# Kernel optimization log

Hardware: AMD Instinct MI355X
Metric: run time of the kernel (lower is better)

Reference implementation:

```python
import jax, jax.numpy as jnp
import numpy as np

B, S, T, K = 96, 4, 16, 36           # groups, fixed 4 slots, max tags per slot, num boxes
V_DIM, Q_DIM, H = 1024, 512, 512


def setup_inputs() -> dict:
    key = jax.random.key(0)
    k_v, k_q, k_m, k_w1, k_b1, k_w2, k_b2 = jax.random.split(key, 7)

    # deterministic ragged lengths in [1, T], cyclic -> sum is exact
    lengths = (np.arange(B * S) % T) + 1              # [B*S], sum = 24 * 136 = 3264
    N = int(lengths.sum())                            # total rows in v / q
    # binary tag-attention mask: first `len` positions set per slot
    tags_attention = (np.arange(T)[None, :] < lengths[:, None]).astype(np.int32)
    tags_attention = jnp.asarray(tags_attention.reshape(B, S, T))

    v = jax.random.normal(k_v, (N, K, V_DIM), dtype=jnp.float32)
    q = jax.random.normal(k_q, (N, Q_DIM), dtype=jnp.float32)

    # box mask: random 0/1 but guarantee at least one valid box per group
    box_mask = (jax.random.uniform(k_m, (B, K)) < 0.9).astype(jnp.float32)
    box_mask = box_mask.at[:, 0].set(1.0)

    # FCNet (weight-normed Linear + ReLU; dropout inactive at eval) and scoring Linear
    w1 = jax.random.normal(k_w1, (V_DIM + Q_DIM, H), dtype=jnp.float32) * 0.02
    b1 = jax.random.normal(k_b1, (H,), dtype=jnp.float32) * 0.02
    w2 = jax.random.normal(k_w2, (H,), dtype=jnp.float32) * 0.02
    b2 = jax.random.normal(k_b2, (), dtype=jnp.float32) * 0.02

    return {"v": v, "q": q, "box_mask": box_mask, "tags_attention": tags_attention,
            "w1": w1, "b1": b1, "w2": w2, "b2": b2}


def reference(v, q, box_mask, tags_attention, w1, b1, w2, b2):
    N, Kb, _ = v.shape
    # logits: concat(v, q repeated over boxes) -> ReLU FC -> scalar score per box
    vq = jnp.concatenate([v, jnp.broadcast_to(q[:, None, :], (N, Kb, q.shape[-1]))], axis=-1)
    joint = jax.nn.relu(jnp.einsum('nkd,dh->nkh', vq, w1) + b1)      # [N, K, H]
    logits = jnp.einsum('nkh,h->nk', joint, w2) + b2                 # [N, K]

    # pad_sequence: ragged rows -> [B, S, T, K] via vectorized gather
    Bg, Sg, Tg = tags_attention.shape
    lengths = tags_attention.sum(-1).reshape(-1)                     # [B*S]
    starts = jnp.cumsum(lengths) - lengths                           # exclusive cumsum
    idx = starts[:, None] + jnp.arange(Tg)                           # [B*S, T]
    valid = jnp.arange(Tg)[None, :] < lengths[:, None]               # [B*S, T]
    gathered = jnp.take(logits, jnp.clip(idx, 0, N - 1), axis=0)     # [B*S, T, K]
    padded = jnp.where(valid[..., None], gathered, 0.0).reshape(Bg, Sg, Tg, Kb)

    # masked_softmax (allennlp-style) over the box dim with box_mask [B,1,1,K]
    mask = box_mask[:, None, None, :]
    s = jax.nn.softmax(padded * mask, axis=-1) * mask
    w = s / (s.sum(axis=-1, keepdims=True) + 1e-13)
    return w
```

## Files before the change

kernel.cpp:

```cpp
#include <hip/hip_runtime.h>
#include <hip/hip_bf16.h>
#include <cstdint>
#include <cstddef>

#define BB 96
#define SS 4
#define TT 16
#define KK 36
#define VDIM 1024
#define QDIM 512
#define HH 512
#define W1R 1536
#define NROWS 3264
#define MM (NROWS * KK)

typedef __attribute__((ext_vector_type(8))) short short8;
typedef __attribute__((ext_vector_type(4))) float f32x4;

static __device__ __forceinline__ unsigned short f2bf(float f) {
    union { float f; unsigned u; } v; v.f = f;
    unsigned u = v.u;
    u += 0x7FFFu + ((u >> 16) & 1u);
    return (unsigned short)(u >> 16);
}

static __device__ __forceinline__ unsigned pk2(float lo, float hi) {
    __hip_bfloat162 h = __float22bfloat162_rn(make_float2(lo, hi));
    union { __hip_bfloat162 h; unsigned u; } cv;
    cv.h = h;
    return cv.u;
}

__device__ __forceinline__ void gload_lds16(const void* g, void* l) {
    __builtin_amdgcn_global_load_lds(
        (const __attribute__((address_space(1))) unsigned int*)g,
        (__attribute__((address_space(3))) unsigned int*)l, 16, 0, 0);
}

#define SB() __builtin_amdgcn_sched_barrier(0)

__global__ __launch_bounds__(256) void prep_w1T(const float* __restrict__ w1,
                                                unsigned short* __restrict__ w1T) {
    __shared__ float tile[64][65];
    int k0 = blockIdx.x * 64;
    int c0 = blockIdx.y * 64;
    int li = threadIdx.x & 63;
    int gi = threadIdx.x >> 6;
#pragma unroll
    for (int r = 0; r < 64; r += 4)
        tile[r + gi][li] = w1[(size_t)(k0 + r + gi) * HH + c0 + li];
    __syncthreads();
#pragma unroll
    for (int r = 0; r < 64; r += 4) {
        int c = r + gi;
        w1T[(size_t)(c0 + c) * W1R + k0 + li] = f2bf(tile[li][c]);
    }
}

__global__ __launch_bounds__(512) void starts_kernel(const int* __restrict__ tags,
                                                     int* __restrict__ starts,
                                                     int* __restrict__ lengths) {
    __shared__ int sl[BB * SS];
    int tid = threadIdx.x;
    int len = 0;
    if (tid < BB * SS) {
#pragma unroll
        for (int i = 0; i < TT; ++i) len += tags[tid * TT + i];
        sl[tid] = len;
    }
    __syncthreads();
    for (int off = 1; off < BB * SS; off <<= 1) {
        int v = 0;
        if (tid < BB * SS && tid >= off) v = sl[tid - off];
        __syncthreads();
        if (tid < BB * SS) sl[tid] += v;
        __syncthreads();
    }
    if (tid < BB * SS) { starts[tid] = sl[tid] - len; lengths[tid] = len; }
}

__global__ __launch_bounds__(256, 3) void qproj_mfma(const float* __restrict__ q,
                                                     const unsigned short* __restrict__ w1T,
                                                     const float* __restrict__ b1,
                                                     float* __restrict__ qp) {
    __shared__ __align__(16) unsigned short At[2][64 * 64];
    __shared__ __align__(16) unsigned short Bt[2][128 * 64];

    int tid = threadIdx.x, lane = tid & 63, wid = tid >> 6;
    int wm = wid >> 1, wn = wid & 1;
    int bx = blockIdx.x;
    int nb = bx & 3, mb = bx >> 2;
    int n0q = mb * 64, cb = nb * 128;
    int lr = lane & 15, lg = lane >> 4;

    const float* a_base = q + (size_t)(n0q + wid * 16 + (lane >> 4)) * QDIM + (lane & 15) * 4;
    const unsigned short* b_base = w1T + (size_t)(cb + wid * 32 + (lane >> 3)) * W1R + 1024
                                 + (((lane & 7) ^ (lane >> 3)) * 8);

    f32x4 acc[2][4];
#pragma unroll
    for (int mt = 0; mt < 2; ++mt)
#pragma unroll
        for (int nt = 0; nt < 4; ++nt) acc[mt][nt] = (f32x4){0.f, 0.f, 0.f, 0.f};

#define QP_CVT_WRITE(DST, AR)                                                  \
    _Pragma("unroll") for (int p = 0; p < 4; ++p) {                            \
        int r = wid * 16 + (lane >> 4) + p * 4;                                \
        int boff = r * 128 + ((((lane & 15) * 8)) ^ ((r & 7) << 4));           \
        uint2 d;                                                               \
        d.x = pk2(AR[p].x, AR[p].y);                                           \
        d.y = pk2(AR[p].z, AR[p].w);                                           \
        *(uint2*)((char*)(DST) + boff) = d;                                    \
    }

#define QP_COMPUTE(AC, BC)                                                     \
    _Pragma("unroll") for (int kk = 0; kk < 2; ++kk) {                         \
        short8 af[2], bf[4];                                                   \
        _Pragma("unroll") for (int mt = 0; mt < 2; ++mt) {                     \
            int R = wm * 32 + mt * 16 + lr;                                    \
            int off = R * 128 + ((kk * 64 + lg * 16) ^ ((R & 7) << 4));        \
            af[mt] = *(const short8*)((const char*)(AC) + off);                \
        }                                                                      \
        _Pragma("unroll") for (int nt = 0; nt < 4; ++nt) {                     \
            int R = wn * 64 + nt * 16 + lr;                                    \
            int off = R * 128 + ((kk * 64 + lg * 16) ^ ((R & 7) << 4));        \
            bf[nt] = *(const short8*)((const char*)(BC) + off);                \
        }                                                                      \
        __builtin_amdgcn_s_setprio(1);                                         \
        _Pragma("unroll") for (int mt = 0; mt < 2; ++mt)                       \
            _Pragma("unroll") for (int nt = 0; nt < 4; ++nt)                   \
                acc[mt][nt] = __builtin_amdgcn_mfma_f32_16x16x32_bf16(         \
                    af[mt], bf[nt], acc[mt][nt], 0, 0, 0);                     \
        __builtin_amdgcn_s_setprio(0);                                         \
    }

    {
        float4 ar[4];
#pragma unroll
        for (int p = 0; p < 4; ++p) ar[p] = *(const float4*)(a_base + (size_t)p * 4 * QDIM);
#pragma unroll
        for (int o = 0; o < 4; ++o)
            gload_lds16(b_base + (size_t)o * 8 * W1R, &Bt[0][(wid * 32 + o * 8) * 64]);
        SB();
        QP_CVT_WRITE(&At[0][0], ar)
    }
#pragma unroll 1
    for (int t = 0; t < 7; ++t) {
        int k0 = (t + 1) * 64;
        const unsigned short* Ac = &At[t & 1][0];
        const unsigned short* Bc = &Bt[t & 1][0];
        unsigned short* An = &At[(t + 1) & 1][0];
        unsigned short* Bn = &Bt[(t + 1) & 1][0];
        float4 ar[4];
#pragma unroll
        for (int p = 0; p < 4; ++p)
            ar[p] = *(const float4*)(a_base + (size_t)p * 4 * QDIM + k0);
#pragma unroll
        for (int o = 0; o < 4; ++o)
            gload_lds16(b_base + (size_t)o * 8 * W1R + k0, &Bn[(wid * 32 + o * 8) * 64]);
        SB();
        asm volatile("s_waitcnt vmcnt(8)" ::: "memory");
        asm volatile("s_waitcnt lgkmcnt(0)" ::: "memory");
        __builtin_amdgcn_s_barrier();
        SB();
        QP_COMPUTE(Ac, Bc)
        SB();
        QP_CVT_WRITE(An, ar)
    }
    SB();
    asm volatile("s_waitcnt vmcnt(0)" ::: "memory");
    asm volatile("s_waitcnt lgkmcnt(0)" ::: "memory");
    __builtin_amdgcn_s_barrier();
    SB();
    QP_COMPUTE(&At[1][0], &Bt[1][0])
#undef QP_COMPUTE
#undef QP_CVT_WRITE

#pragma unroll
    for (int nt = 0; nt < 4; ++nt) {
        int c = cb + wn * 64 + nt * 16 + lr;
        float b1v = b1[c];
#pragma unroll
        for (int mt = 0; mt < 2; ++mt)
#pragma unroll
            for (int r = 0; r < 4; ++r) {
                int row = wm * 32 + mt * 16 + lg * 4 + r;
                qp[(size_t)(n0q + row) * HH + c] = acc[mt][nt][r] + b1v;
            }
    }
}

__global__ __launch_bounds__(512, 2) void main_gemm(const float* __restrict__ v,
                                                    const unsigned short* __restrict__ w1T,
                                                    const float* __restrict__ qp,
                                                    const float* __restrict__ w2,
                                                    float* __restrict__ logits2) {
    __shared__ __align__(16) unsigned short At[2][16384];
    __shared__ __align__(16) unsigned short Bt[2][16384];

    int tid = threadIdx.x, lane = tid & 63, wid = tid >> 6;
    int wm = wid >> 2, wn = wid & 3;
    int bx = blockIdx.x;
    int xcd = bx & 7;
    int base = (xcd < 6) ? xcd * 115 : 690 + (xcd - 6) * 114;
    int orig = base + (bx >> 3);
    int ch = orig & 1, mb = orig >> 1;
    int m0 = mb * 256, cb = ch * 256;
    int lr = lane & 15, lg = lane >> 4;

    const float* a_base = v + (size_t)(m0 + wid * 32 + (lane >> 4)) * VDIM + (lane & 15) * 4;
    const unsigned short* b_base = w1T + (size_t)(cb + wid * 32 + (lane >> 3)) * W1R
                                 + (((lane & 7) ^ (lane >> 3)) * 8);

    f32x4 acc[8][4];
#pragma unroll
    for (int mt = 0; mt < 8; ++mt)
#pragma unroll
        for (int nt = 0; nt < 4; ++nt) acc[mt][nt] = (f32x4){0.f, 0.f, 0.f, 0.f};

#define MG_CVT_WRITE(AN, AR)                                                   \
    _Pragma("unroll") for (int p = 0; p < 8; ++p) {                            \
        int r = wid * 32 + (lane >> 4) + p * 4;                                \
        int boff = r * 128 + ((((lane & 15) * 8)) ^ ((r & 7) << 4));           \
        uint2 d;                                                               \
        d.x = pk2(AR[p].x, AR[p].y);                                           \
        d.y = pk2(AR[p].z, AR[p].w);                                           \
        *(uint2*)((char*)(AN) + boff) = d;                                     \
    }

#define MG_READ_A8(AF, AC, MTB)                                                \
    _Pragma("unroll") for (int mt = 0; mt < 4; ++mt)                           \
        _Pragma("unroll") for (int kk = 0; kk < 2; ++kk) {                     \
            int R = wm * 128 + ((MTB) + mt) * 16 + lr;                         \
            int off = R * 128 + ((kk * 64 + lg * 16) ^ ((R & 7) << 4));        \
            AF[mt * 2 + kk] = *(const short8*)((const char*)(AC) + off);       \
        }

#define MG_READ_B8(BF, BC)                                                     \
    _Pragma("unroll") for (int nt = 0; nt < 4; ++nt)                           \
        _Pragma("unroll") for (int kk = 0; kk < 2; ++kk) {                     \
            int C = wn * 64 + nt * 16 + lr;                                    \
            int off = C * 128 + ((kk * 64 + lg * 16) ^ ((C & 7) << 4));        \
            BF[nt * 2 + kk] = *(const short8*)((const char*)(BC) + off);       \
        }

#define MG_MFMA32(AF, BF, MTB)                                                 \
    __builtin_amdgcn_s_setprio(1);                                             \
    _Pragma("unroll") for (int mt = 0; mt < 4; ++mt)                           \
        _Pragma("unroll") for (int nt = 0; nt < 4; ++nt)                       \
            _Pragma("unroll") for (int kk = 0; kk < 2; ++kk)                   \
                acc[(MTB) + mt][nt] = __builtin_amdgcn_mfma_f32_16x16x32_bf16( \
                    AF[mt * 2 + kk], BF[nt * 2 + kk], acc[(MTB) + mt][nt],     \
                    0, 0, 0);                                                  \
    __builtin_amdgcn_s_setprio(0);

#define BODY(T, AC, AN, BC, BN, VM)                                            \
  do {                                                                         \
    float4 ar[8];                                                              \
    if ((T) < 15) {                                                            \
        const int kA = ((T) + 1) * 64;                                         \
        _Pragma("unroll") for (int p = 0; p < 8; ++p)                          \
            ar[p] = *(const float4*)(a_base + (size_t)p * 4 * VDIM + kA);      \
    }                                                                          \
    SB();                                                                      \
    asm volatile("s_waitcnt vmcnt(" VM ")" ::: "memory");     \
    asm volatile("s_waitcnt lgkmcnt(0)" ::: "memory");    \
    __builtin_amdgcn_s_barrier();                                              \
    SB();                                                                      \
    if ((T) < 15) {       \
        const int kB = ((T) + 1) * 64;                                         \
        _Pragma("unroll") for (int o = 0; o < 4; ++o)                          \
            gload_lds16(b_base + (size_t)o * 8 * W1R + kB,                     \
                        (BN) + (wid * 32 + o * 8) * 64);                       \
    }                                                                          \
    SB();                                                                      \
    {                                                                          \
        short8 af0[8], bfv[8];                                                 \
        MG_READ_A8(af0, AC, 0)                                                 \
        MG_READ_B8(bfv, BC)                                                    \
        MG_MFMA32(af0, bfv, 0)                                                 \
        short8 af1[8];                                                         \
        MG_READ_A8(af1, AC, 4)                                                 \
        MG_MFMA32(af1, bfv, 4)                                                 \
    }                                                                          \
    SB();                                                                      \
    if ((T) < 15) { MG_CVT_WRITE(AN, ar) }         \
  } while (0)

    {
        float4 ar[8];
#pragma unroll
        for (int p = 0; p < 8; ++p) ar[p] = *(const float4*)(a_base + (size_t)p * 4 * VDIM);
#pragma unroll
        for (int o = 0; o < 4; ++o)
            gload_lds16(b_base + (size_t)o * 8 * W1R, &Bt[0][(wid * 32 + o * 8) * 64]);
        SB();
        MG_CVT_WRITE(At[0], ar)
    }

#pragma unroll 1
    for (int tt = 0; tt < 14; tt += 2) {
        BODY(tt,     At[0], At[1], Bt[0], Bt[1], "8");
        BODY(tt + 1, At[1], At[0], Bt[1], Bt[0], "8");
    }
    BODY(14, At[0], At[1], Bt[0], Bt[1], "8");
    BODY(15, At[1], At[0], Bt[1], Bt[0], "0");
#undef BODY
#undef MG_MFMA32
#undef MG_READ_A8
#undef MG_READ_B8
#undef MG_CVT_WRITE

    __syncthreads();
    float* qs = (float*)&At[0][0];
    float* fl = qs + 9 * 256;
    int n0 = m0 / KK;
    for (int i = tid; i < 9 * 256; i += 512) {
        int nn = n0 + (i >> 8);
        if (nn >= NROWS) nn = NROWS - 1;
        qs[i] = qp[(size_t)nn * HH + cb + (i & 255)];
    }
    __syncthreads();

    float part[8][4] = {{0.f}};
#pragma unroll
    for (int nt = 0; nt < 4; ++nt) {
        int c = wn * 64 + nt * 16 + lr;
        float w2v = w2[cb + c];
#pragma unroll
        for (int mt = 0; mt < 8; ++mt)
#pragma unroll
            for (int r = 0; r < 4; ++r) {
                int row = wm * 128 + mt * 16 + lg * 4 + r;
                int ni = (m0 + row) / KK - n0;
                float pre = acc[mt][nt][r] + qs[ni * 256 + c];
                part[mt][r] += fmaxf(pre, 0.f) * w2v;
            }
    }
#pragma unroll
    for (int mt = 0; mt < 8; ++mt)
#pragma unroll
        for (int r = 0; r < 4; ++r) {
            float s = part[mt][r];
            s += __shfl_xor(s, 1, 64);
            s += __shfl_xor(s, 2, 64);
            s += __shfl_xor(s, 4, 64);
            s += __shfl_xor(s, 8, 64);
            if (lr == 0) fl[wn * 256 + wm * 128 + mt * 16 + lg * 4 + r] = s;
        }
    __syncthreads();
    if (tid < 256)
        logits2[(size_t)ch * MM + m0 + tid] =
            fl[tid] + fl[256 + tid] + fl[512 + tid] + fl[768 + tid];
}

__global__ __launch_bounds__(256) void softmax_kernel(const float* __restrict__ logits2,
                                                      const float* __restrict__ box_mask,
                                                      const int* __restrict__ starts,
                                                      const int* __restrict__ lengths,
                                                      float* __restrict__ out) {
    int lane = threadIdx.x & 63;
    int g = blockIdx.x * 4 + (threadIdx.x >> 6);
    int t   = g & (TT - 1);
    int row = g >> 4;
    int b   = row >> 2;

    int length = lengths[row];
    int start  = starts[row];

    int k = lane;
    bool kv = k < KK;
    float mval = kv ? box_mask[b * KK + k] : 0.f;
    bool act = kv && (mval != 0.f);

    float l = 0.f;
    if (act && t < length) {
        size_t idx = (size_t)(start + t) * KK + k;
        l = logits2[idx] + logits2[MM + idx];
    }

    float lm = act ? l : -1e30f;
#pragma unroll
    for (int off = 32; off >= 1; off >>= 1) lm = fmaxf(lm, __shfl_xor(lm, off, 64));

    float e = act ? expf(l - lm) : 0.f;
    float se = e;
#pragma unroll
    for (int off = 32; off >= 1; off >>= 1) se += __shfl_xor(se, off, 64);

    if (kv) out[(size_t)g * KK + k] = e / se;
}

extern "C" void kernel_launch(void* const* d_in, const int* in_sizes, int n_in,
                              void* d_out, int out_size, void* d_ws, size_t ws_size,
                              hipStream_t stream) {
    const float* v        = (const float*)d_in[0];
    const float* q        = (const float*)d_in[1];
    const float* box_mask = (const float*)d_in[2];
    const int*   tags     = (const int*)d_in[3];
    const float* w1       = (const float*)d_in[4];
    const float* b1       = (const float*)d_in[5];
    const float* w2       = (const float*)d_in[6];

    char* ws = (char*)d_ws;
    unsigned short* w1T   = (unsigned short*)ws;
    float* qp      = (float*)(ws + 1572864);
    float* logits2 = (float*)(ws + 1572864 + 6684672);
    int*   starts  = (int*)(ws + 1572864 + 6684672 + 940032);
    int*   lengths = (int*)(ws + 1572864 + 6684672 + 940032 + 1536);
    float* out     = (float*)d_out;

    hipLaunchKernelGGL(prep_w1T, dim3(24, 8), dim3(256), 0, stream, w1, w1T);
    hipLaunchKernelGGL(starts_kernel, dim3(1), dim3(512), 0, stream, tags, starts, lengths);
    hipLaunchKernelGGL(qproj_mfma, dim3((NROWS / 64) * 4), dim3(256), 0, stream,
                       q, w1T, b1, qp);
    hipLaunchKernelGGL(main_gemm, dim3((MM / 256) * 2), dim3(512), 0, stream,
                       v, w1T, qp, w2, logits2);
    hipLaunchKernelGGL(softmax_kernel, dim3((BB * SS * TT) / 4), dim3(256), 0, stream,
                       logits2, box_mask, starts, lengths, out);
}
```

Before: 252.4 us.

## Restructure GEMM main loop into eight-phase ping-pong schedule with split prefetches

```diff
diff --git a/kernel.cpp b/kernel.cpp
--- a/kernel.cpp
+++ b/kernel.cpp
@@ -218,6 +218,12 @@
 #pragma unroll
         for (int nt = 0; nt < 4; ++nt) acc[mt][nt] = (f32x4){0.f, 0.f, 0.f, 0.f};
 
+    float4 ar[8];
+
+#define MG_LOADA(AR, KA)                                                       \
+    _Pragma("unroll") for (int p = 0; p < 8; ++p)                              \
+        AR[p] = *(const float4*)(a_base + (size_t)p * 4 * VDIM + (KA));
+
 #define MG_CVT_WRITE(AN, AR)                                                   \
     _Pragma("unroll") for (int p = 0; p < 8; ++p) {                            \
         int r = wid * 32 + (lane >> 4) + p * 4;                                \
@@ -228,14 +234,6 @@
         *(uint2*)((char*)(AN) + boff) = d;                                     \
     }
 
-#define MG_READ_A8(AF, AC, MTB)                                                \
-    _Pragma("unroll") for (int mt = 0; mt < 4; ++mt)                           \
-        _Pragma("unroll") for (int kk = 0; kk < 2; ++kk) {                     \
-            int R = wm * 128 + ((MTB) + mt) * 16 + lr;                         \
-            int off = R * 128 + ((kk * 64 + lg * 16) ^ ((R & 7) << 4));        \
-            AF[mt * 2 + kk] = *(const short8*)((const char*)(AC) + off);       \
-        }
-
 #define MG_READ_B8(BF, BC)                                                     \
     _Pragma("unroll") for (int nt = 0; nt < 4; ++nt)                           \
         _Pragma("unroll") for (int kk = 0; kk < 2; ++kk) {                     \
@@ -244,72 +242,127 @@
             BF[nt * 2 + kk] = *(const short8*)((const char*)(BC) + off);       \
         }
 
-#define MG_MFMA32(AF, BF, MTB)                                                 \
+#define MG_READ_AQ(AF, AC, Q)                                                  \
+    _Pragma("unroll") for (int j = 0; j < 2; ++j)                              \
+        _Pragma("unroll") for (int kk = 0; kk < 2; ++kk) {                     \
+            int R = wm * 128 + (2 * (Q) + j) * 16 + lr;                        \
+            int off = R * 128 + ((kk * 64 + lg * 16) ^ ((R & 7) << 4));        \
+            AF[j * 2 + kk] = *(const short8*)((const char*)(AC) + off);        \
+        }
+
+#define MG_MFMA16(AF, BFV, Q)                                                  \
     __builtin_amdgcn_s_setprio(1);                                             \
-    _Pragma("unroll") for (int mt = 0; mt < 4; ++mt)                           \
+    _Pragma("unroll") for (int j = 0; j < 2; ++j)                              \
         _Pragma("unroll") for (int nt = 0; nt < 4; ++nt)                       \
             _Pragma("unroll") for (int kk = 0; kk < 2; ++kk)                   \
-                acc[(MTB) + mt][nt] = __builtin_amdgcn_mfma_f32_16x16x32_bf16( \
-                    AF[mt * 2 + kk], BF[nt * 2 + kk], acc[(MTB) + mt][nt],     \
-                    0, 0, 0);                                                  \
+                acc[2 * (Q) + j][nt] =                                         \
+                    __builtin_amdgcn_mfma_f32_16x16x32_bf16(                   \
+                        AF[j * 2 + kk], BFV[nt * 2 + kk],                      \
+                        acc[2 * (Q) + j][nt], 0, 0, 0);                        \
     __builtin_amdgcn_s_setprio(0);
 
-#define BODY(T, AC, AN, BC, BN, VM)                                            \
+#define PH_SYNC()                                                              \
+    SB(); __builtin_amdgcn_s_barrier();                                        \
+    asm volatile("s_waitcnt lgkmcnt(0)" ::: "memory"); SB();
+
+#define PH_END() SB(); __builtin_amdgcn_s_barrier();
+
+#define BDMA2(BN, KB, O0, O1)                                                  \
+    gload_lds16(b_base + (size_t)(O0) * 8 * W1R + (KB),                        \
+                (BN) + (wid * 32 + (O0) * 8) * 64);                            \
+    gload_lds16(b_base + (size_t)(O1) * 8 * W1R + (KB),                        \
+                (BN) + (wid * 32 + (O1) * 8) * 64);
+
+#define ITER(T0, F, L)                                                         \
   do {                                                                         \
-    float4 ar[8];                                                              \
-    if ((T) < 15) {                                                            \
-        const int kA = ((T) + 1) * 64;                                         \
-        _Pragma("unroll") for (int p = 0; p < 8; ++p)                          \
-            ar[p] = *(const float4*)(a_base + (size_t)p * 4 * VDIM + kA);      \
-    }                                                                          \
-    SB();                                                                      \
-    asm volatile("s_waitcnt vmcnt(" VM ")" ::: "memory");     \
-    asm volatile("s_waitcnt lgkmcnt(0)" ::: "memory");    \
-    __builtin_amdgcn_s_barrier();                                              \
-    SB();                                                                      \
-    if ((T) < 15) {       \
-        const int kB = ((T) + 1) * 64;                                         \
-        _Pragma("unroll") for (int o = 0; o < 4; ++o)                          \
-            gload_lds16(b_base + (size_t)o * 8 * W1R + kB,                     \
-                        (BN) + (wid * 32 + o * 8) * 64);                       \
-    }                                                                          \
-    SB();                                                                      \
-    {                                                                          \
-        short8 af0[8], bfv[8];                                                 \
-        MG_READ_A8(af0, AC, 0)                                                 \
-        MG_READ_B8(bfv, BC)                                                    \
-        MG_MFMA32(af0, bfv, 0)                                                 \
-        short8 af1[8];                                                         \
-        MG_READ_A8(af1, AC, 4)                                                 \
-        MG_MFMA32(af1, bfv, 4)                                                 \
-    }                                                                          \
-    SB();                                                                      \
-    if ((T) < 15) { MG_CVT_WRITE(AN, ar) }         \
+    short8 bfv[8];                                                             \
+    {                   \
+      if (!(F)) { MG_CVT_WRITE(At[1], ar) }                                    \
+      short8 af[4];                                                            \
+      MG_READ_B8(bfv, Bt[0])                                                   \
+      MG_READ_AQ(af, At[0], 0)                                                 \
+      PH_SYNC() MG_MFMA16(af, bfv, 0) PH_END()                                 \
+    }                                                                          \
+    {                 \
+      if (!(L)) { MG_LOADA(ar, ((T0) + 2) * 64) }                              \
+      short8 af[4]; MG_READ_AQ(af, At[0], 1)                                   \
+      if (!(L)) { BDMA2(Bt[0], ((T0) + 2) * 64, 0, 1) }                        \
+      PH_SYNC() MG_MFMA16(af, bfv, 1) PH_END()                                 \
+    }                                                                          \
+    {                                               \
+      short8 af[4]; MG_READ_AQ(af, At[0], 2)                                   \
+      if (!(L)) { BDMA2(Bt[0], ((T0) + 2) * 64, 2, 3) }                        \
+      PH_SYNC() MG_MFMA16(af, bfv, 2) PH_END()                                 \
+    }                                                                          \
+    {                                \
+      short8 af[4]; MG_READ_AQ(af, At[0], 3)                                   \
+      SB();                                                                    \
+      if (!(L)) { asm volatile("s_waitcnt vmcnt(12)" ::: "memory"); }          \
+      else      { asm volatile("s_waitcnt vmcnt(0)"  ::: "memory"); }          \
+      PH_SYNC() MG_MFMA16(af, bfv, 3) PH_END()                                 \
+    }                                                                          \
+    {                   \
+      short8 af[4];                                                            \
+      MG_READ_B8(bfv, Bt[1])                                                   \
+      MG_READ_AQ(af, At[1], 0)                                                 \
+      if (!(L)) { MG_CVT_WRITE(At[0], ar) }                                    \
+      PH_SYNC() MG_MFMA16(af, bfv, 0) PH_END()                                 \
+    }                                                                          \
+    {                 \
+      if (!(L)) { MG_LOADA(ar, ((T0) + 3) * 64) }                              \
+      short8 af[4]; MG_READ_AQ(af, At[1], 1)                                   \
+      if (!(L)) { BDMA2(Bt[1], ((T0) + 3) * 64, 0, 1) }                        \
+      PH_SYNC() MG_MFMA16(af, bfv, 1) PH_END()                                 \
+    }                                                                          \
+    {                                               \
+      short8 af[4]; MG_READ_AQ(af, At[1], 2)                                   \
+      if (!(L)) { BDMA2(Bt[1], ((T0) + 3) * 64, 2, 3) }                        \
+      PH_SYNC() MG_MFMA16(af, bfv, 2) PH_END()                                 \
+    }                                                                          \
+    {                              \
+      short8 af[4]; MG_READ_AQ(af, At[1], 3)                                   \
+      SB();                                                                    \
+      if (!(L)) { asm volatile("s_waitcnt vmcnt(12)" ::: "memory"); }          \
+      else      { asm volatile("s_waitcnt vmcnt(0)"  ::: "memory"); }          \
+      PH_SYNC() MG_MFMA16(af, bfv, 3) PH_END()                                 \
+    }                                                                          \
   } while (0)
 
     {
-        float4 ar[8];
-#pragma unroll
-        for (int p = 0; p < 8; ++p) ar[p] = *(const float4*)(a_base + (size_t)p * 4 * VDIM);
 #pragma unroll
         for (int o = 0; o < 4; ++o)
             gload_lds16(b_base + (size_t)o * 8 * W1R, &Bt[0][(wid * 32 + o * 8) * 64]);
+        MG_LOADA(ar, 0)
         SB();
         MG_CVT_WRITE(At[0], ar)
-    }
-
+        MG_LOADA(ar, 64)
+        SB();
+        MG_CVT_WRITE(At[1], ar)
+#pragma unroll
+        for (int o = 0; o < 4; ++o)
+            gload_lds16(b_base + (size_t)o * 8 * W1R + 64, &Bt[1][(wid * 32 + o * 8) * 64]);
+        SB();
+        asm volatile("s_waitcnt lgkmcnt(0)" ::: "memory");
+        __builtin_amdgcn_s_barrier();
+        SB();
+    }
+
+    ITER(0, 1, 0);
 #pragma unroll 1
-    for (int tt = 0; tt < 14; tt += 2) {
-        BODY(tt,     At[0], At[1], Bt[0], Bt[1], "8");
-        BODY(tt + 1, At[1], At[0], Bt[1], Bt[0], "8");
-    }
-    BODY(14, At[0], At[1], Bt[0], Bt[1], "8");
-    BODY(15, At[1], At[0], Bt[1], Bt[0], "0");
-#undef BODY
-#undef MG_MFMA32
-#undef MG_READ_A8
+    for (int ii = 1; ii < 7; ++ii) {
+        int t0 = ii * 2;
+        ITER(t0, 0, 0);
+    }
+    ITER(14, 0, 1);
+#undef ITER
+#undef BDMA2
+#undef PH_END
+#undef PH_SYNC
+#undef MG_MFMA16
+#undef MG_READ_AQ
 #undef MG_READ_B8
 #undef MG_CVT_WRITE
+#undef MG_LOADA
 
     __syncthreads();
     float* qs = (float*)&At[0][0];
```

Measured after the change: 324.4 us. 28.5% more time.
